# Performance work log

Hardware: AMD Instinct MI355X
Metric: run time of the kernel (lower is better)

Reference implementation:

```python
import jax, jax.numpy as jnp
import numpy as np

EMBED_DIM = 512
NHEAD = 8
HEAD_DIM = EMBED_DIM // NHEAD
NEG_INF = -1e8
U, B, R, S, M = 1024, 16, 256, 32, 31
Q = R + U + S   # 1312
KV = M + R + U  # 1311


def setup_inputs() -> dict:
    key = jax.random.key(0)
    ks = jax.random.split(key, 12)
    f = lambda k, shp: jax.random.normal(k, shp, dtype=jnp.float32)
    s = 1.0 / np.sqrt(EMBED_DIM)
    return {
        "utterance": f(ks[0], (U, B, EMBED_DIM)),
        "right_context": f(ks[1], (R, B, EMBED_DIM)),
        "summary": f(ks[2], (S, B, EMBED_DIM)),
        "memory": f(ks[3], (M, B, EMBED_DIM)),
        "attention_mask": jax.random.randint(ks[4], (Q, KV), 0, 2).astype(bool),
        "padding_mask": jax.random.randint(ks[5], (B, KV), 0, 2).astype(bool),
        "Wq": f(ks[6], (EMBED_DIM, EMBED_DIM)) * s,
        "bq": f(ks[7], (EMBED_DIM,)) * 0.1,
        "Wkv": f(ks[8], (2 * EMBED_DIM, EMBED_DIM)) * s,
        "bkv": f(ks[9], (2 * EMBED_DIM,)) * 0.1,
        "Wo": f(ks[10], (EMBED_DIM, EMBED_DIM)) * s * 0.25,
        "bo": f(ks[11], (EMBED_DIM,)) * 0.1,
    }


def reference(utterance, right_context, summary, memory, attention_mask,
              padding_mask, Wq, bq, Wkv, bkv, Wo, bo):
    scaling = HEAD_DIM ** -0.5
    # query = [right_context, utterance, summary]  -> (Q, B, D)
    q_in = jnp.concatenate([right_context, utterance, summary], axis=0)
    # key/value = [memory, right_context, utterance] -> (KV, B, D)
    kv_in = jnp.concatenate([memory, right_context, utterance], axis=0)
    query = q_in @ Wq.T + bq
    kv = kv_in @ Wkv.T + bkv
    key_t, value = jnp.split(kv, 2, axis=2)

    def heads(t):  # (L, B, D) -> (B*nhead, L, head_dim)
        return t.reshape(t.shape[0], B * NHEAD, HEAD_DIM).transpose(1, 0, 2)

    qh = heads(query) * scaling
    kh = heads(key_t)
    vh = heads(value)
    # (B*nhead, Q, KV) attention scores in float32 (matches .float() cast)
    w = jnp.einsum('bqd,bkd->bqk', qh, kh).astype(jnp.float32)
    w = jnp.where(attention_mask[None], NEG_INF, w)
    w = w.reshape(B, NHEAD, Q, KV)
    w = jnp.where(padding_mask[:, None, None, :], NEG_INF, w)
    probs = jax.nn.softmax(w.reshape(B * NHEAD, Q, KV), axis=-1)
    # dropout p=0.0 -> identity
    attn = jnp.einsum('bqk,bkd->bqd', probs, vh)  # (B*nhead, Q, head_dim)
    attn = attn.transpose(1, 0, 2).reshape(Q, B, EMBED_DIM)
    out = attn @ Wo.T + bo
    output_right_context_utterance = out[:R + U]
    # tanh_on_mem=False -> clamp to [-10, 10]; forward returns memory[:-1]
    output_memory = jnp.clip(out[R + U:], -10.0, 10.0)[:-1]
    return output_right_context_utterance, output_memory
```

## Files before the change

### kernel.cpp

```cpp
#include <hip/hip_runtime.h>
#include <hip/hip_bf16.h>

#define EMBED 512
#define NHEAD 8
#define HDIM  64
#define B_    16
#define U_    1024
#define R_    256
#define S_    32
#define M_    31
#define Q_    (R_ + U_ + S_)
#define KV_   (M_ + R_ + U_)

#define QROWS  (Q_ * B_)
#define KVROWS (KV_ * B_)
#define OROWS  (1311 * B_)
#define OUT0_ROWS (1280 * B_)

#define KVPAD_ROWS 1344
#define KPAD 1344
#define MROWSTRIDE 44

#define QSCALE 0.18033688011112042f
#define SOFF  16.0f
#define MASKV (-40.0f)

typedef __attribute__((ext_vector_type(8))) short bf16x8;
typedef __attribute__((ext_vector_type(4))) short short4v;
typedef __attribute__((ext_vector_type(4))) float f32x4;
#define MFMA16(a, b, c) __builtin_amdgcn_mfma_f32_16x16x32_bf16(a, b, c, 0, 0, 0)

typedef unsigned short ushort_t;

__device__ __forceinline__ ushort_t f2bf(float x) {
    __hip_bfloat16 h = __float2bfloat16(x);
    return *reinterpret_cast<ushort_t*>(&h);
}
__device__ __forceinline__ float bf2f(ushort_t h) {
    return __uint_as_float((unsigned)h << 16);
}
__device__ __forceinline__ float exp2_raw(float x) {
    return __builtin_amdgcn_exp2f(x);
}

__device__ __forceinline__ void gload_lds16(const void* g, void* l) {
    __builtin_amdgcn_global_load_lds(
        (const __attribute__((address_space(1))) unsigned int*)g,
        (__attribute__((address_space(3))) unsigned int*)l, 16, 0, 0);
}

__global__ __launch_bounds__(256) void cvt_all(
    const float* __restrict__ s0, const float* __restrict__ s1,
    const float* __restrict__ s2, const float* __restrict__ s3,
    const float* __restrict__ s4, const float* __restrict__ s5,
    const float* __restrict__ s6,
    ushort_t* __restrict__ SRC_hi, ushort_t* __restrict__ W_hi,
    const int* __restrict__ am, const int* __restrict__ pm,
    unsigned* __restrict__ am_p, unsigned* __restrict__ pm_p)
{
    int bid = blockIdx.x;
    if (bid >= 5884) {
        const int NA = Q_ * MROWSTRIDE;
        const int NP = B_ * MROWSTRIDE;
        int idx = (bid - 5884) * 256 + threadIdx.x;
        if (idx < NA) {
            int q = idx / MROWSTRIDE, w_ = idx % MROWSTRIDE;
            unsigned bits = 0xFFFFFFFFu;
            if (w_ < 41) {
                bits = 0;
                #pragma unroll 4
                for (int i = 0; i < 32; ++i) {
                    int kg = w_ * 32 + i;
                    int v = (kg < KV_) ? am[(size_t)q * KV_ + kg] : 1;
                    bits |= (unsigned)(v != 0) << i;
                }
            }
            am_p[idx] = bits;
        } else if (idx < NA + NP) {
            int j = idx - NA;
            int bb = j / MROWSTRIDE, w_ = j % MROWSTRIDE;
            unsigned bits = 0xFFFFFFFFu;
            if (w_ < 41) {
                bits = 0;
                #pragma unroll 4
                for (int i = 0; i < 32; ++i) {
                    int kg = w_ * 32 + i;
                    int v = (kg < KV_) ? pm[bb * KV_ + kg] : 1;
                    bits |= (unsigned)(v != 0) << i;
                }
            }
            pm_p[j] = bits;
        }
        return;
    }

    const float* src; ushort_t* hi; int n8;
    if (bid < 4096)      { src = s0; hi = SRC_hi;            n8 = 1048576; }
    else if (bid < 5120) { src = s1; hi = SRC_hi + 8388608;  n8 = 262144; bid -= 4096; }
    else if (bid < 5248) { src = s2; hi = SRC_hi + 10485760; n8 = 32768;  bid -= 5120; }
    else if (bid < 5372) { src = s3; hi = SRC_hi + 10747904; n8 = 31744;  bid -= 5248; }
    else if (bid < 5500) { src = s4; hi = W_hi;              n8 = 32768;  bid -= 5372; }
    else if (bid < 5756) { src = s5; hi = W_hi + 262144;     n8 = 65536;  bid -= 5500; }
    else                 { src = s6; hi = W_hi + 786432;     n8 = 32768;  bid -= 5756; }

    int i = bid * 256 + threadIdx.x;
    if (i >= n8) return;
    const float4* s = (const float4*)(src + (size_t)i * 8);
    float4 a = s[0], b2 = s[1];
    float xs[8] = {a.x, a.y, a.z, a.w, b2.x, b2.y, b2.z, b2.w};
    bf16x8 hv;
    #pragma unroll
    for (int j = 0; j < 8; ++j) hv[j] = (short)f2bf(xs[j]);
    *(bf16x8*)(hi + (size_t)i * 8) = hv;
}

__global__ __launch_bounds__(256) void vtrans(
    const ushort_t* __restrict__ Vp, ushort_t* __restrict__ VT)
{
    __shared__ ushort_t Lt[64][72];
    const int tid = threadIdx.x;
    const int kt  = blockIdx.x;
    const int bh  = blockIdx.y;
    const int b   = bh >> 3, h = bh & 7;
    const int sub = tid >> 3;
    const int g   = tid & 7;

    #pragma unroll
    for (int p = 0; p < 2; ++p) {
        int k = kt * 64 + p * 32 + sub;
        bf16x8 v;
        if (k < KV_) {
            v = *(const bf16x8*)(Vp + ((size_t)k * B_ + b) * EMBED + h * HDIM + g * 8);
        } else {
            #pragma unroll
            for (int j = 0; j < 8; ++j) v[j] = 0;
        }
        #pragma unroll
        for (int j = 0; j < 8; ++j)
            Lt[g * 8 + j][p * 32 + sub] = (ushort_t)v[j];
    }
    __syncthreads();
    #pragma unroll
    for (int p = 0; p < 2; ++p) {
        int d = p * 32 + sub;
        bf16x8 v = *(const bf16x8*)&Lt[d][g * 8];
        if (d & 8) {
            bf16x8 t;
            #pragma unroll
            for (int j = 0; j < 8; ++j) t[j] = v[j ^ 4];
            v = t;
        }
        *(bf16x8*)(VT + ((size_t)(bh * 64 + d)) * KPAD + kt * 64 + g * 8) = v;
    }
}

template<int MODE>
__global__ __launch_bounds__(256) void gemm_mfma(
    const ushort_t* __restrict__ A, const ushort_t* __restrict__ W,
    const float* __restrict__ bias, float scale,
    int n0, int n01, int nrows,
    size_t off0, size_t off1, size_t off2,
    void* __restrict__ o0, void* __restrict__ o1, void* __restrict__ o2)
{
    __shared__ __align__(16) ushort_t lA[128][64];
    __shared__ __align__(16) ushort_t lW[128][64];

    const int tid = threadIdx.x;
    const int w   = tid >> 6;
    const int l   = tid & 63;
    const int l15 = l & 15;
    const int l4  = l >> 4;
    const int row0 = blockIdx.x * 128;
    const int col0 = blockIdx.y * 128;

    const int drow = l >> 3;
    const int sgr  = (l & 7) ^ drow;
    const ushort_t* aptr[4];
    const ushort_t* wptr[4];
    #pragma unroll
    for (int c = 0; c < 4; ++c) {
        int r = row0 + w * 32 + c * 8 + drow;
        int rc = r < nrows ? r : nrows - 1;
        size_t roff;
        if (MODE == 2)      roff = (size_t)rc * EMBED;
        else if (rc < n0)   roff = off0 + (size_t)rc * EMBED;
        else if (rc < n01)  roff = off1 + (size_t)(rc - n0) * EMBED;
        else                roff = off2 + (size_t)(rc - n01) * EMBED;
        aptr[c] = A + roff + sgr * 8;
        int wr = col0 + w * 32 + c * 8 + drow;
        wptr[c] = W + (size_t)wr * EMBED + sgr * 8;
    }

    f32x4 acc[4][4];
    #pragma unroll
    for (int mi = 0; mi < 4; ++mi)
        #pragma unroll
        for (int nj = 0; nj < 4; ++nj) acc[mi][nj] = (f32x4){0.f, 0.f, 0.f, 0.f};

    const int wrow = (w >> 1) * 64;
    const int wcol = (w & 1) * 64;

    for (int t = 0; t < 8; ++t) {
        __syncthreads();
        const int ke = t * 64;
        #pragma unroll
        for (int c = 0; c < 4; ++c) {
            gload_lds16(aptr[c] + ke, &lA[w * 32 + c * 8][0]);
            gload_lds16(wptr[c] + ke, &lW[w * 32 + c * 8][0]);
        }
        __syncthreads();

        #pragma unroll
        for (int kk = 0; kk < 2; ++kk) {
            bf16x8 ah[4], wh[4];
            #pragma unroll
            for (int mi = 0; mi < 4; ++mi) {
                int row = wrow + mi * 16 + l15;
                int g = (((kk * 4 + l4) ^ (l15 & 7))) * 8;
                ah[mi] = *(const bf16x8*)&lA[row][g];
            }
            #pragma unroll
            for (int nj = 0; nj < 4; ++nj) {
                int row = wcol + nj * 16 + l15;
                int g = (((kk * 4 + l4) ^ (l15 & 7))) * 8;
                wh[nj] = *(const bf16x8*)&lW[row][g];
            }
            #pragma unroll
            for (int mi = 0; mi < 4; ++mi)
                #pragma unroll
                for (int nj = 0; nj < 4; ++nj)
                    acc[mi][nj] = MFMA16(ah[mi], wh[nj], acc[mi][nj]);
        }
    }

    #pragma unroll
    for (int nj = 0; nj < 4; ++nj) {
        int gc = col0 + wcol + nj * 16 + l15;
        float bv = bias[gc];
        #pragma unroll
        for (int mi = 0; mi < 4; ++mi) {
            #pragma unroll
            for (int r = 0; r < 4; ++r) {
                int gr = row0 + wrow + mi * 16 + l4 * 4 + r;
                if (gr >= nrows) continue;
                float v = (acc[mi][nj][r] + bv) * scale;
                if (MODE == 0) {
                    ((ushort_t*)o0)[(size_t)gr * EMBED + gc] = f2bf(v);
                } else if (MODE == 1) {
                    if (gc < EMBED)
                        ((ushort_t*)o0)[(size_t)gr * EMBED + gc] = f2bf(v);
                    else
                        ((ushort_t*)o2)[(size_t)gr * EMBED + (gc - EMBED)] = f2bf(v);
                } else {
                    if (gr < OUT0_ROWS)
                        ((float*)o0)[(size_t)gr * EMBED + gc] = v;
                    else if (gr < OROWS)
                        ((float*)o1)[(size_t)(gr - OUT0_ROWS) * EMBED + gc] =
                            fminf(fmaxf(v, -10.f), 10.f);
                }
            }
        }
    }
}

__global__ __launch_bounds__(512, 4) void attn_mfma(
    const ushort_t* __restrict__ Q_p,
    const ushort_t* __restrict__ Khi_p, const ushort_t* __restrict__ VT,
    const unsigned* __restrict__ am_p, const unsigned* __restrict__ pm_p,
    ushort_t* __restrict__ C_p)
{
    __shared__ __align__(16) ushort_t SM[16384];
    #define KlAt(buf, row) (SM + (buf) * 4096 + (row) * 64)
    #define VtAt(buf, row) (SM + 8192 + (buf) * 4096 + (row) * 64)

    const int tid = threadIdx.x;
    const int w   = tid >> 6;
    const int l   = tid & 63;
    const int l15 = l & 15;
    const int l4  = l >> 4;
    const int q0  = blockIdx.x * 128;
    const int bh  = blockIdx.y;
    const int b   = bh >> 3, h = bh & 7;

    bf16x8 Qf[2];
    {
        int qa = q0 + w * 16 + l15;
        if (qa >= Q_) qa = Q_ - 1;
        size_t base = ((size_t)qa * B_ + b) * EMBED + h * HDIM;
        #pragma unroll
        for (int dh = 0; dh < 2; ++dh)
            Qf[dh] = *(const bf16x8*)(Q_p + base + dh * 32 + l4 * 8);
    }

    bf16x8 ONES;
    #pragma unroll
    for (int j = 0; j < 8; ++j) ONES[j] = (l15 == 0) ? (short)0x3F80 : (short)0;

    const unsigned* awp;
    {
        int q = q0 + w * 16 + l15;
        if (q >= Q_) q = Q_ - 1;
        awp = am_p + (size_t)q * MROWSTRIDE;
    }
    const unsigned* pwp = pm_p + b * MROWSTRIDE;

    const int krl  = l >> 3;
    const int gsrc = (l & 7) ^ krl;
    const int srow = w * 8 + krl;

    const ushort_t* kSrc0 =
        Khi_p + ((size_t)srow * B_ + b) * EMBED + h * HDIM + gsrc * 8;
    const ushort_t* vSrc0 =
        VT + ((size_t)(bh * 64 + srow)) * KPAD + gsrc * 8;

    const int gb  = l4 >> 1;
    const int hsw = ((l4 & 1) ^ ((l15 >> 3) & 1)) * 4;
    const int x7  = l15 & 7;

    f32x4 SS = (f32x4){0.f, 0.f, 0.f, 0.f};
    f32x4 O[4];
    #pragma unroll
    for (int dg = 0; dg < 4; ++dg) O[dg] = (f32x4){0.f, 0.f, 0.f, 0.f};

    auto stage = [&](int kbase, int buf) {
        gload_lds16(kSrc0 + (size_t)kbase * B_ * EMBED, KlAt(buf, w * 8));
        gload_lds16(vSrc0 + kbase, VtAt(buf, w * 8));
    };

    stage(0, 0);
    __syncthreads();
    int cur = 0;

    for (int kt = 0; kt < 21; ++kt) {
        uint2 pw  = *(const uint2*)&pwp[2 * kt];
        uint2 awv = *(const uint2*)&awp[2 * kt];
        unsigned m0 = (awv.x | pw.x) >> (l4 * 4);
        unsigned m1 = (awv.y | pw.y) >> (l4 * 4);

        if (kt < 20) stage((kt + 1) * 64, cur ^ 1);

        f32x4 S[4];
        __builtin_amdgcn_s_setprio(1);
        #pragma unroll
        for (int c = 0; c < 4; ++c) {
            f32x4 acc = (f32x4){0.f, 0.f, 0.f, 0.f};
            int krow = c * 16 + l15;
            #pragma unroll
            for (int dh = 0; dh < 2; ++dh) {
                int gr = ((dh * 4 + l4) ^ (krow & 7)) * 8;
                bf16x8 Bh = *(const bf16x8*)(KlAt(cur, krow) + gr);
                acc = MFMA16(Bh, Qf[dh], acc);
            }
            S[c] = acc;
        }
        __builtin_amdgcn_s_setprio(0);

        bf16x8 PB[2];
        #pragma unroll
        for (int c = 0; c < 4; ++c) {
            unsigned mw = (c & 2) ? m1 : m0;
            int sh = (c & 1) << 4;
            #pragma unroll
            for (int r = 0; r < 4; ++r) {
                float s = ((mw >> (sh + r)) & 1) ? MASKV : S[c][r];
                PB[c >> 1][(c & 1) * 4 + r] = (short)f2bf(exp2_raw(s - SOFF));
            }
        }

        __builtin_amdgcn_s_setprio(1);
        SS = MFMA16(ONES, PB[0], SS);
        SS = MFMA16(ONES, PB[1], SS);
        #pragma unroll
        for (int kh = 0; kh < 2; ++kh) {
            #pragma unroll
            for (int dg = 0; dg < 4; ++dg) {
                int rw = dg * 16 + l15;
                const ushort_t* vrow = VtAt(cur, rw);
                int G0 = (kh * 4 + gb) ^ x7;
                int G1 = (kh * 4 + 2 + gb) ^ x7;
                union { bf16x8 v8; short4v h2[2]; } u;
                u.h2[0] = *(const short4v*)(vrow + G0 * 8 + hsw);
                u.h2[1] = *(const short4v*)(vrow + G1 * 8 + hsw);
                O[dg] = MFMA16(u.v8, PB[kh], O[dg]);
            }
        }
        __builtin_amdgcn_s_setprio(0);

        __syncthreads();
        cur ^= 1;
    }

    float sT  = __shfl(SS[0], l15, 64);
    float inv = 1.f / sT;

    float* TB = ((float*)SM) + w * 1024;
    #pragma unroll
    for (int dg = 0; dg < 4; ++dg) {
        f32x4 vv;
        #pragma unroll
        for (int r = 0; r < 4; ++r) vv[r] = O[dg][r] * inv;
        int gsw = (dg * 4 + l4) ^ (l15 & 7);
        *(f32x4*)(TB + l15 * 64 + gsw * 4) = vv;
    }

    #pragma unroll
    for (int qq = 0; qq < 16; ++qq) {
        int q = q0 + w * 16 + qq;
        if (q >= Q_) break;
        float v = TB[qq * 64 + (((l >> 2) ^ (qq & 7)) * 4) + (l & 3)];
        size_t off = ((size_t)q * B_ + b) * EMBED + h * HDIM + l;
        C_p[off] = f2bf(v);
    }
    #undef KlAt
    #undef VtAt
}

extern "C" void kernel_launch(void* const* d_in, const int* in_sizes, int n_in,
                              void* d_out, int out_size, void* d_ws, size_t ws_size,
                              hipStream_t stream) {
    const float* utter = (const float*)d_in[0];
    const float* rctx  = (const float*)d_in[1];
    const float* summ  = (const float*)d_in[2];
    const float* mem   = (const float*)d_in[3];
    const int* amask   = (const int*)d_in[4];
    const int* pmask   = (const int*)d_in[5];
    const float* Wq  = (const float*)d_in[6];
    const float* bq  = (const float*)d_in[7];
    const float* Wkv = (const float*)d_in[8];
    const float* bkv = (const float*)d_in[9];
    const float* Wo  = (const float*)d_in[10];
    const float* bo  = (const float*)d_in[11];

    const size_t UT_OFF = 0;
    const size_t RC_OFF = 8388608;
    const size_t SM_OFF = 10485760;
    const size_t MM_OFF = 10747904;
    const size_t SRC_N  = 11001856;
    const size_t WQ_OFF = 0, WKV_OFF = 262144, WO_OFF = 786432;
    const size_t W_N = 1048576;
    const size_t KVPLANE = (size_t)KVPAD_ROWS * B_ * EMBED;

    ushort_t* p = (ushort_t*)d_ws;
    ushort_t* SRC_hi = p;                p += SRC_N;
    ushort_t* Wp_hi  = p;                p += W_N;
    ushort_t* Q_p    = p;                p += (size_t)QROWS * EMBED;
    ushort_t* Khi_p  = p;                p += KVPLANE;
    ushort_t* VT_p   = p;                p += KVPLANE;
    ushort_t* Vp     = p;                p += KVPLANE;
    ushort_t* C_p    = p;                p += (size_t)QROWS * EMBED;
    unsigned* am_p   = (unsigned*)p;     p += (size_t)2 * KVPAD_ROWS * MROWSTRIDE;
    unsigned* pm_p   = (unsigned*)p;     p += (size_t)2 * B_ * MROWSTRIDE;

    float* out0 = (float*)d_out;
    float* out1 = out0 + (size_t)OUT0_ROWS * EMBED;

    dim3 blk(256);

    cvt_all<<<dim3(6113), blk, 0, stream>>>(
        utter, rctx, summ, mem, Wq, Wkv, Wo,
        SRC_hi, Wp_hi, amask, pmask, am_p, pm_p);

    gemm_mfma<0><<<dim3(QROWS / 128, EMBED / 128), blk, 0, stream>>>(
        SRC_hi, Wp_hi + WQ_OFF, bq, QSCALE,
        R_ * B_, (R_ + U_) * B_, QROWS, RC_OFF, UT_OFF, SM_OFF,
        Q_p, nullptr, nullptr);

    gemm_mfma<1><<<dim3((KVROWS + 127) / 128, (2 * EMBED) / 128), blk, 0, stream>>>(
        SRC_hi, Wp_hi + WKV_OFF, bkv, 1.0f,
        M_ * B_, (M_ + R_) * B_, KVROWS, MM_OFF, RC_OFF, UT_OFF,
        Khi_p, nullptr, Vp);

    vtrans<<<dim3(21, 128), blk, 0, stream>>>(Vp, VT_p);

    attn_mfma<<<dim3((Q_ + 127) / 128, B_ * NHEAD), dim3(512), 0, stream>>>(
        Q_p, Khi_p, VT_p, am_p, pm_p, C_p);

    gemm_mfma<2><<<dim3(QROWS / 128, EMBED / 128), blk, 0, stream>>>(
        C_p, Wp_hi + WO_OFF, bo, 1.0f,
        QROWS, QROWS, QROWS, 0, 0, 0,
        out0, out1, nullptr);
}
```

Before: 285.6 us.

## Double attention KV tile to 128 keys and fold softmax offset into accumulator init

The attention kernel now processes 128 keys per iteration instead of 64. That halves the loop trips and block-wide barriers, and doubles the LDS buffers to 64KB. The V-transpose padding grows to 1408 and vtrans gets an extra block column to cover the larger final tile. The fixed softmax shift is moved into the QK accumulator's initial value, which removes a subtract per element. The risks are lower occupancy from the doubled LDS and more wasted padded keys in the last tile.

New measurement: 285.1 us. Within noise of the previous version (-0.2%).

```diff
diff --git a/kernel.cpp b/kernel.cpp
--- a/kernel.cpp
+++ b/kernel.cpp
@@ -17,13 +17,13 @@
 #define OROWS  (1311 * B_)
 #define OUT0_ROWS (1280 * B_)
 
-#define KVPAD_ROWS 1344
-#define KPAD 1344
+#define KVPAD_ROWS 1408
+#define KPAD 1408
 #define MROWSTRIDE 44
 
 #define QSCALE 0.18033688011112042f
-#define SOFF  16.0f
-#define MASKV (-40.0f)
+#define SOFFI (-16.0f)
+#define MASKV (-56.0f)
 
 typedef __attribute__((ext_vector_type(8))) short bf16x8;
 typedef __attribute__((ext_vector_type(4))) short short4v;
@@ -269,9 +269,9 @@
     const unsigned* __restrict__ am_p, const unsigned* __restrict__ pm_p,
     ushort_t* __restrict__ C_p)
 {
-    __shared__ __align__(16) ushort_t SM[16384];
-    #define KlAt(buf, row) (SM + (buf) * 4096 + (row) * 64)
-    #define VtAt(buf, row) (SM + 8192 + (buf) * 4096 + (row) * 64)
+    __shared__ __align__(16) ushort_t SM[32768];
+    #define KlAt(buf, row) (SM + (buf) * 8192 + (row) * 64)
+    #define VtAt(buf, row) (SM + 16384 + (buf) * 8192 + (row) * 128)
 
     const int tid = threadIdx.x;
     const int w   = tid >> 6;
@@ -304,14 +304,17 @@
     }
     const unsigned* pwp = pm_p + b * MROWSTRIDE;
 
-    const int krl  = l >> 3;
-    const int gsrc = (l & 7) ^ krl;
-    const int srow = w * 8 + krl;
-
+    const int krl = l >> 3;
+    const int gsK = (l & 7) ^ krl;
     const ushort_t* kSrc0 =
-        Khi_p + ((size_t)srow * B_ + b) * EMBED + h * HDIM + gsrc * 8;
-    const ushort_t* vSrc0 =
-        VT + ((size_t)(bh * 64 + srow)) * KPAD + gsrc * 8;
+        Khi_p + ((size_t)(w * 8 + krl) * B_ + b) * EMBED + h * HDIM + gsK * 8;
+
+    const int vro = l >> 4;
+    const int g16 = l & 15;
+    const ushort_t* vSrcA =
+        VT + ((size_t)(bh * 64 + w * 8 + vro)) * KPAD + ((g16 ^ vro) * 8);
+    const ushort_t* vSrcB =
+        VT + ((size_t)(bh * 64 + w * 8 + 4 + vro)) * KPAD + ((g16 ^ (4 + vro)) * 8);
 
     const int gb  = l4 >> 1;
     const int hsw = ((l4 & 1) ^ ((l15 >> 3) & 1)) * 4;
@@ -323,31 +326,38 @@
     for (int dg = 0; dg < 4; ++dg) O[dg] = (f32x4){0.f, 0.f, 0.f, 0.f};
 
     auto stage = [&](int kbase, int buf) {
-        gload_lds16(kSrc0 + (size_t)kbase * B_ * EMBED, KlAt(buf, w * 8));
-        gload_lds16(vSrc0 + kbase, VtAt(buf, w * 8));
+        gload_lds16(kSrc0 + (size_t)kbase * B_ * EMBED,        KlAt(buf, w * 8));
+        gload_lds16(kSrc0 + (size_t)(kbase + 64) * B_ * EMBED, KlAt(buf, 64 + w * 8));
+        gload_lds16(vSrcA + kbase, VtAt(buf, w * 8));
+        gload_lds16(vSrcB + kbase, VtAt(buf, w * 8 + 4));
     };
 
     stage(0, 0);
     __syncthreads();
     int cur = 0;
 
-    for (int kt = 0; kt < 21; ++kt) {
-        uint2 pw  = *(const uint2*)&pwp[2 * kt];
-        uint2 awv = *(const uint2*)&awp[2 * kt];
-        unsigned m0 = (awv.x | pw.x) >> (l4 * 4);
-        unsigned m1 = (awv.y | pw.y) >> (l4 * 4);
-
-        if (kt < 20) stage((kt + 1) * 64, cur ^ 1);
-
-        f32x4 S[4];
+    for (int kt = 0; kt < 11; ++kt) {
+        uint2 pw0 = *(const uint2*)&pwp[4 * kt];
+        uint2 pw1 = *(const uint2*)&pwp[4 * kt + 2];
+        uint2 aw0 = *(const uint2*)&awp[4 * kt];
+        uint2 aw1 = *(const uint2*)&awp[4 * kt + 2];
+        unsigned mm[4];
+        mm[0] = (aw0.x | pw0.x) >> (l4 * 4);
+        mm[1] = (aw0.y | pw0.y) >> (l4 * 4);
+        mm[2] = (aw1.x | pw1.x) >> (l4 * 4);
+        mm[3] = (aw1.y | pw1.y) >> (l4 * 4);
+
+        if (kt < 10) stage((kt + 1) * 128, cur ^ 1);
+
+        f32x4 S[8];
         __builtin_amdgcn_s_setprio(1);
         #pragma unroll
-        for (int c = 0; c < 4; ++c) {
-            f32x4 acc = (f32x4){0.f, 0.f, 0.f, 0.f};
+        for (int c = 0; c < 8; ++c) {
+            f32x4 acc = (f32x4){SOFFI, SOFFI, SOFFI, SOFFI};
             int krow = c * 16 + l15;
             #pragma unroll
             for (int dh = 0; dh < 2; ++dh) {
-                int gr = ((dh * 4 + l4) ^ (krow & 7)) * 8;
+                int gr = ((dh * 4 + l4) ^ x7) * 8;
                 bf16x8 Bh = *(const bf16x8*)(KlAt(cur, krow) + gr);
                 acc = MFMA16(Bh, Qf[dh], acc);
             }
@@ -355,23 +365,25 @@
         }
         __builtin_amdgcn_s_setprio(0);
 
-        bf16x8 PB[2];
-        #pragma unroll
-        for (int c = 0; c < 4; ++c) {
-            unsigned mw = (c & 2) ? m1 : m0;
+        bf16x8 PB[4];
+        #pragma unroll
+        for (int c = 0; c < 8; ++c) {
+            unsigned mw = mm[c >> 1];
             int sh = (c & 1) << 4;
             #pragma unroll
             for (int r = 0; r < 4; ++r) {
                 float s = ((mw >> (sh + r)) & 1) ? MASKV : S[c][r];
-                PB[c >> 1][(c & 1) * 4 + r] = (short)f2bf(exp2_raw(s - SOFF));
+                PB[c >> 1][(c & 1) * 4 + r] = (short)f2bf(exp2_raw(s));
             }
         }
 
         __builtin_amdgcn_s_setprio(1);
         SS = MFMA16(ONES, PB[0], SS);
         SS = MFMA16(ONES, PB[1], SS);
-        #pragma unroll
-        for (int kh = 0; kh < 2; ++kh) {
+        SS = MFMA16(ONES, PB[2], SS);
+        SS = MFMA16(ONES, PB[3], SS);
+        #pragma unroll
+        for (int kh = 0; kh < 4; ++kh) {
             #pragma unroll
             for (int dg = 0; dg < 4; ++dg) {
                 int rw = dg * 16 + l15;
@@ -470,7 +482,7 @@
         M_ * B_, (M_ + R_) * B_, KVROWS, MM_OFF, RC_OFF, UT_OFF,
         Khi_p, nullptr, Vp);
 
-    vtrans<<<dim3(21, 128), blk, 0, stream>>>(Vp, VT_p);
+    vtrans<<<dim3(22, 128), blk, 0, stream>>>(Vp, VT_p);
 
     attn_mfma<<<dim3((Q_ + 127) / 128, B_ * NHEAD), dim3(512), 0, stream>>>(
         Q_p, Khi_p, VT_p, am_p, pm_p, C_p);
```
